# Optimization experiments

Measured on AMD Instinct MI355X. Metric: run time of the kernel, lower is better.

## Reference

```python
import jax, jax.numpy as jnp
import numpy as np

B, T, N, H = 256, 256, 512, 512  # batch, seq_len, input_size, hidden_size_encoder


def setup_inputs() -> dict:
    key = jax.random.key(0)
    k = jax.random.split(key, 9)
    return {
        "input_data": jax.random.normal(k[0], (B, T, N), dtype=jnp.float32),
        # init_hidden uses xavier_normal on zeros -> random init; std ~ sqrt(2/(B+H))
        "h0": jax.random.normal(k[1], (B, H), dtype=jnp.float32) * 0.06,
        "c0": jax.random.normal(k[2], (B, H), dtype=jnp.float32) * 0.06,
        # attn Linear: in_features = 2H + T, out_features = 1
        "attn_w": jax.random.normal(k[3], (2 * H + T,), dtype=jnp.float32) * 0.02,
        "attn_b": jnp.zeros((), dtype=jnp.float32),
        # single-layer LSTM params (torch gate order: i, f, g, o)
        "w_ih": jax.random.normal(k[4], (4 * H, N), dtype=jnp.float32) * 0.02,
        "w_hh": jax.random.normal(k[5], (4 * H, H), dtype=jnp.float32) * 0.02,
        "b_ih": jax.random.normal(k[6], (4 * H,), dtype=jnp.float32) * 0.02,
        "b_hh": jax.random.normal(k[7], (4 * H,), dtype=jnp.float32) * 0.02,
    }


def reference(input_data, h0, c0, attn_w, attn_b, w_ih, w_hh, b_ih, b_hh):
    Bd, Td, Nd = input_data.shape
    Hd = h0.shape[-1]
    # split attn weight into h-, c-, and x-parts (same math as the concat+Linear)
    w_h, w_c, w_x = attn_w[:Hd], attn_w[Hd:2 * Hd], attn_w[2 * Hd:]
    # x-part of the attention logits is time-invariant: [B, N]
    proj_x = jnp.einsum('btn,t->bn', input_data, w_x)
    b_gate = b_ih + b_hh  # [4H]

    def step(carry, x_t):  # x_t: [B, N]
        h, c = carry
        # attention logits: broadcast h/c contribution over the N input series
        e = proj_x + (h @ w_h)[:, None] + (c @ w_c)[:, None] + attn_b  # [B, N]
        a = jax.nn.softmax(e, axis=1)  # softmax over input_size dim
        weighted = a * x_t  # [B, N]
        gates = weighted @ w_ih.T + h @ w_hh.T + b_gate  # [B, 4H]
        i_g, f_g, g_g, o_g = jnp.split(gates, 4, axis=1)
        i_g = jax.nn.sigmoid(i_g)
        f_g = jax.nn.sigmoid(f_g)
        g_g = jnp.tanh(g_g)
        o_g = jax.nn.sigmoid(o_g)
        c_new = f_g * c + i_g * g_g
        h_new = o_g * jnp.tanh(c_new)
        return (h_new, c_new), (a, h_new)

    xs = jnp.swapaxes(input_data, 0, 1)  # [T, B, N]
    _, (attn_seq, enc_seq) = jax.lax.scan(step, (h0, c0), xs)
    attentions = jnp.swapaxes(attn_seq, 0, 1)      # [B, T, N]
    input_encoded = jnp.swapaxes(enc_seq, 0, 1)    # [B, T, H]
    return attentions, input_encoded
```

## Files before the change

kernel.cpp:

```cpp
#include <hip/hip_runtime.h>

#define BB 256
#define TT 256
#define NN 512
#define HH 512

typedef short short8 __attribute__((ext_vector_type(8)));
typedef float f32x4 __attribute__((ext_vector_type(4)));
typedef unsigned long long u64;

static __device__ __forceinline__ ushort f2bf(float f) {
  uint b = __builtin_bit_cast(uint, f);
  b += 0x7FFFu + ((b >> 16) & 1u);
  return (ushort)(b >> 16);
}
static __device__ __forceinline__ uint pk2(float lo, float hi) {
  return (uint)f2bf(lo) | ((uint)f2bf(hi) << 16);
}
static __device__ __forceinline__ float sigm_(float x) {
  return 1.0f / (1.0f + exp2f(-1.4426950408889634f * x));
}
static __device__ __forceinline__ float tanh_(float x) {
  return 2.0f / (1.0f + exp2f(-2.8853900817779268f * x)) - 1.0f;
}
static __device__ __forceinline__ void bar_lds() {
  asm volatile("s_waitcnt lgkmcnt(0)" ::: "memory");
  __builtin_amdgcn_s_barrier();
}

__global__ __launch_bounds__(256) void prep_kernel(
    const float* __restrict__ w_ih, const float* __restrict__ w_hh,
    const float* __restrict__ b_ih, const float* __restrict__ b_hh,
    const float* __restrict__ h0,
    ushort* __restrict__ W2, float* __restrict__ bgate,
    uint* __restrict__ hx16a, unsigned* __restrict__ bar) {
  int idx = blockIdx.x * 256 + threadIdx.x;
  if (idx < 2048 * 1024) {
    int row = idx >> 10;
    int k = idx & 1023;
    float v = (k < NN) ? w_ih[row * NN + k] : w_hh[row * HH + (k - NN)];
    W2[idx] = f2bf(v);
  }
  if (idx < 2048) bgate[idx] = b_ih[idx] + b_hh[idx];
  if (idx < BB * HH / 2) hx16a[idx] = pk2(h0[2 * idx], h0[2 * idx + 1]);
  if (idx < 16 * 64) bar[idx] = 0u;
}

__global__ __launch_bounds__(256) void attn_kernel(
    const float* __restrict__ x, const float* __restrict__ attn_w,
    float* __restrict__ a_out, ushort* __restrict__ ax) {
  __shared__ float wx[TT];
  __shared__ float as[NN];
  __shared__ float red[8];
  const int b = blockIdx.x;
  const int tid = threadIdx.x;
  wx[tid] = attn_w[2 * HH + tid];
  __syncthreads();

  const float* xb = x + (size_t)b * TT * NN;
  float p0 = 0.0f, p1 = 0.0f;
  for (int t = 0; t < TT; ++t) {
    float w = wx[t];
    p0 += xb[t * NN + tid] * w;
    p1 += xb[t * NN + 256 + tid] * w;
  }

  const int lane = tid & 63, wv = tid >> 6;
  float m = fmaxf(p0, p1);
  #pragma unroll
  for (int o = 32; o; o >>= 1) m = fmaxf(m, __shfl_xor(m, o));
  if (lane == 0) red[wv] = m;
  __syncthreads();
  m = fmaxf(fmaxf(red[0], red[1]), fmaxf(red[2], red[3]));
  float e0 = expf(p0 - m), e1 = expf(p1 - m);
  float s = e0 + e1;
  #pragma unroll
  for (int o = 32; o; o >>= 1) s += __shfl_xor(s, o);
  if (lane == 0) red[4 + wv] = s;
  __syncthreads();
  s = red[4] + red[5] + red[6] + red[7];
  float inv = 1.0f / s;
  float a0 = e0 * inv, a1 = e1 * inv;
  a_out[b * NN + tid] = a0;
  a_out[b * NN + 256 + tid] = a1;
  as[tid] = a0;
  as[tid + 256] = a1;
  __syncthreads();

  const float aa0 = as[tid * 2], aa1 = as[tid * 2 + 1];
  ushort* axb = ax + (size_t)b * TT * NN;
  for (int t = 0; t < TT; ++t) {
    const float2 xv = *(const float2*)(xb + t * NN + tid * 2);
    *(uint*)(axb + t * NN + tid * 2) = pk2(aa0 * xv.x, aa1 * xv.y);
  }
}

__global__ __launch_bounds__(256) void bcast_kernel(
    const float* __restrict__ a, float* __restrict__ attn_out) {
  const size_t idx = (size_t)blockIdx.x * 256 + threadIdx.x;
  const int n4 = (int)(idx & 127);
  const int t = (int)((idx >> 7) & 255);
  const int b = (int)(idx >> 15);
  const float4 v = *(const float4*)(a + b * NN + n4 * 4);
  *(float4*)(attn_out + (((size_t)b * TT + t) * NN + n4 * 4)) = v;
}

__global__ __launch_bounds__(512, 2) void lstm_persistent(
    const ushort* __restrict__ ax,
    const ushort* __restrict__ W2,
    const float* __restrict__ bgate,
    const float* __restrict__ c0,
    uint* __restrict__ hx16a, uint* __restrict__ hx16b,
    float* __restrict__ enc,
    unsigned* __restrict__ bar) {
  __shared__ ushort hx[16 * 1024];
  __shared__ unsigned warr;
  __shared__ unsigned step_flag;

  const int tid = threadIdx.x;
  const int lane = tid & 63;
  const int w = tid >> 6;
  const int bg = blockIdx.x & 15;
  const int jt = blockIdx.x >> 4;
  const int gb0 = bg * 16;
  unsigned* const barp = bar + bg * 64;

  if (tid == 0) { warr = 0u; step_flag = 0u; }

  f32x4 areg[32];
  {
    const int r = lane & 15;
    const int grow = (r & 3) * 512 + jt * 32 + w * 4 + (r >> 2);
    const ushort* wp = W2 + (size_t)grow * 1024 + ((lane >> 4) << 3);
    #pragma unroll
    for (int i = 0; i < 32; ++i) {
      areg[i] = *(const f32x4*)(wp + (i << 5));
      asm volatile("" : "+v"(areg[i]));
    }
  }

  const int srow = tid >> 5;
  const int sl = tid & 31;
  const int r7 = srow & 7;

  const int eb = lane & 15;
  const int kq = lane >> 4;
  const int ecol = jt * 32 + w * 4 + kq;
  const float bgi = bgate[ecol];
  const float bgf = bgate[512 + ecol];
  const float bgg = bgate[1024 + ecol];
  const float bgo = bgate[1536 + ecol];
  float c_reg = c0[(size_t)(gb0 + eb) * HH + ecol];

  const int bbase = (lane & 15) * 1024;
  const int br7 = (lane & 15) & 7;

  uint4 px0, px1;
  {
    const ushort* axp = ax + ((size_t)(gb0 + srow) * TT + 0) * NN;
    px0 = *(const uint4*)(axp + sl * 8);
    px1 = *(const uint4*)(axp + 256 + sl * 8);
  }

  for (int t = 0; t < TT; ++t) {
    const uint* hin = (t & 1) ? hx16b : hx16a;
    uint* hout = (t & 1) ? hx16a : hx16b;

    *(uint4*)&hx[srow * 1024 + ((sl ^ r7) << 3)] = px0;
    *(uint4*)&hx[srow * 1024 + (((32 + sl) ^ r7) << 3)] = px1;
    if (t + 1 < TT) {
      const ushort* axp = ax + ((size_t)(gb0 + srow) * TT + (t + 1)) * NN;
      px0 = *(const uint4*)(axp + sl * 8);
      px1 = *(const uint4*)(axp + 256 + sl * 8);
    }
    bar_lds();

    f32x4 acc = {0.f, 0.f, 0.f, 0.f};
    u64 q0, q1, q2, q3;
    const uint* hrow = hin + (size_t)(gb0 + srow) * 256;

    auto xmfma = [&]() {
      #pragma unroll
      for (int ks = 0; ks < 16; ++ks) {
        const int ag = ks * 4 + kq;
        const short8 bf = *(const short8*)&hx[bbase + ((ag ^ br7) << 3)];
        acc = __builtin_amdgcn_mfma_f32_16x16x32_bf16(
            __builtin_bit_cast(short8, areg[ks]), bf, acc, 0, 0, 0);
      }
    };
    auto hload = [&]() {
      q0 = __hip_atomic_load((const u64*)(hrow + sl * 4),
                             __ATOMIC_RELAXED, __HIP_MEMORY_SCOPE_AGENT);
      q1 = __hip_atomic_load((const u64*)(hrow + sl * 4 + 2),
                             __ATOMIC_RELAXED, __HIP_MEMORY_SCOPE_AGENT);
      q2 = __hip_atomic_load((const u64*)(hrow + 128 + sl * 4),
                             __ATOMIC_RELAXED, __HIP_MEMORY_SCOPE_AGENT);
      q3 = __hip_atomic_load((const u64*)(hrow + 128 + sl * 4 + 2),
                             __ATOMIC_RELAXED, __HIP_MEMORY_SCOPE_AGENT);
    };

    if (t == 0) {
      hload();
      xmfma();
    } else if (w == 0) {
      if (lane == 0) {
        const unsigned target = 16u * (unsigned)t;
        while (__hip_atomic_load(barp, __ATOMIC_RELAXED,
                                 __HIP_MEMORY_SCOPE_AGENT) < target)
          __builtin_amdgcn_s_sleep(1);
        __hip_atomic_store(&step_flag, (unsigned)t, __ATOMIC_RELEASE,
                           __HIP_MEMORY_SCOPE_WORKGROUP);
      }
      asm volatile("" ::: "memory");
      hload();
      xmfma();
    } else {
      xmfma();
      if (lane == 0) {
        while (__hip_atomic_load(&step_flag, __ATOMIC_ACQUIRE,
                                 __HIP_MEMORY_SCOPE_WORKGROUP) < (unsigned)t) {}
      }
      asm volatile("" ::: "memory");
      hload();
    }

    {
      uint4 p0, p1;
      p0.x = (uint)q0; p0.y = (uint)(q0 >> 32);
      p0.z = (uint)q1; p0.w = (uint)(q1 >> 32);
      p1.x = (uint)q2; p1.y = (uint)(q2 >> 32);
      p1.z = (uint)q3; p1.w = (uint)(q3 >> 32);
      *(uint4*)&hx[srow * 1024 + (((64 + sl) ^ r7) << 3)] = p0;
      *(uint4*)&hx[srow * 1024 + (((96 + sl) ^ r7) << 3)] = p1;
    }
    bar_lds();

    #pragma unroll
    for (int ks = 16; ks < 32; ++ks) {
      const int ag = ks * 4 + kq;
      const short8 bf = *(const short8*)&hx[bbase + ((ag ^ br7) << 3)];
      acc = __builtin_amdgcn_mfma_f32_16x16x32_bf16(
          __builtin_bit_cast(short8, areg[ks]), bf, acc, 0, 0, 0);
    }

    {
      const float ig = sigm_(acc[0] + bgi);
      const float fg = sigm_(acc[1] + bgf);
      const float gg = tanh_(acc[2] + bgg);
      const float og = sigm_(acc[3] + bgo);
      const float cn = fg * c_reg + ig * gg;
      const float hn = og * tanh_(cn);
      c_reg = cn;
      const float hp_ = __shfl_xor(hn, 16);
      if (!(lane & 16)) {
        __hip_atomic_store(hout + (size_t)(gb0 + eb) * 256 + (ecol >> 1),
                           pk2(hn, hp_),
                           __ATOMIC_RELAXED, __HIP_MEMORY_SCOPE_AGENT);
      }
      asm volatile("s_waitcnt vmcnt(0)" ::: "memory");
      if (lane == 0) {
        const unsigned old = __hip_atomic_fetch_add(
            &warr, 1u, __ATOMIC_ACQ_REL, __HIP_MEMORY_SCOPE_WORKGROUP);
        if (old == 8u * (unsigned)t + 7u)
          __hip_atomic_fetch_add(barp, 1u, __ATOMIC_RELAXED,
                                 __HIP_MEMORY_SCOPE_AGENT);
      }
      enc[((size_t)(gb0 + eb) * TT + t) * HH + ecol] = hn;
    }
  }
}

extern "C" void kernel_launch(void* const* d_in, const int* in_sizes, int n_in,
                              void* d_out, int out_size, void* d_ws, size_t ws_size,
                              hipStream_t stream) {
  const float* x      = (const float*)d_in[0];
  const float* h0     = (const float*)d_in[1];
  const float* c0     = (const float*)d_in[2];
  const float* attn_w = (const float*)d_in[3];
  const float* w_ih   = (const float*)d_in[5];
  const float* w_hh   = (const float*)d_in[6];
  const float* b_ih   = (const float*)d_in[7];
  const float* b_hh   = (const float*)d_in[8];

  float* attn_out = (float*)d_out;
  float* enc_out  = (float*)d_out + (size_t)BB * TT * NN;
  ushort* ax = (ushort*)d_out;

  char* ws = (char*)d_ws;
  float*    a_ws  = (float*)(ws);
  ushort*   W2_ws = (ushort*)(ws + 0x80000);
  float*    bg_ws = (float*)(ws + 0x480000);
  uint*     hx16a = (uint*)(ws + 0x482000);
  uint*     hx16b = (uint*)(ws + 0x4C2000);
  unsigned* bar   = (unsigned*)(ws + 0x502000);

  prep_kernel<<<8192, 256, 0, stream>>>(w_ih, w_hh, b_ih, b_hh, h0,
                                        W2_ws, bg_ws, hx16a, bar);
  attn_kernel<<<BB, 256, 0, stream>>>(x, attn_w, a_ws, ax);

  {
    dim3 grid(256), block(512);
    void* args[] = {(void*)&ax, (void*)&W2_ws, (void*)&bg_ws, (void*)&c0,
                    (void*)&hx16a, (void*)&hx16b, (void*)&enc_out,
                    (void*)&bar};
    hipLaunchCooperativeKernel((void*)lstm_persistent, grid, block, args, 0,
                               stream);
  }

  bcast_kernel<<<32768, 256, 0, stream>>>(a_ws, attn_out);
}
```

Measured before the change: 833.2 us.

## Double-buffer LDS x tile to drop per-step barrier and split x-MFMA around h wait

Measured after the change: 1.220 ms. 46.5% more time.

```diff
diff --git a/kernel.cpp b/kernel.cpp
--- a/kernel.cpp
+++ b/kernel.cpp
@@ -113,7 +113,7 @@
     uint* __restrict__ hx16a, uint* __restrict__ hx16b,
     float* __restrict__ enc,
     unsigned* __restrict__ bar) {
-  __shared__ ushort hx[16 * 1024];
+  __shared__ ushort hx[2][16 * 1024];
   __shared__ unsigned warr;
   __shared__ unsigned step_flag;
 
@@ -124,8 +124,6 @@
   const int jt = blockIdx.x >> 4;
   const int gb0 = bg * 16;
   unsigned* const barp = bar + bg * 64;
-
-  if (tid == 0) { warr = 0u; step_flag = 0u; }
 
   f32x4 areg[32];
   {
@@ -158,70 +156,74 @@
   uint4 px0, px1;
   {
     const ushort* axp = ax + ((size_t)(gb0 + srow) * TT + 0) * NN;
-    px0 = *(const uint4*)(axp + sl * 8);
-    px1 = *(const uint4*)(axp + 256 + sl * 8);
-  }
+    const uint4 a0 = *(const uint4*)(axp + sl * 8);
+    const uint4 a1 = *(const uint4*)(axp + 256 + sl * 8);
+    *(uint4*)&hx[0][srow * 1024 + ((sl ^ r7) << 3)] = a0;
+    *(uint4*)&hx[0][srow * 1024 + (((32 + sl) ^ r7) << 3)] = a1;
+    const ushort* axp1 = ax + ((size_t)(gb0 + srow) * TT + 1) * NN;
+    px0 = *(const uint4*)(axp1 + sl * 8);
+    px1 = *(const uint4*)(axp1 + 256 + sl * 8);
+  }
+  if (tid == 0) { warr = 0u; step_flag = 0u; }
+  __syncthreads();
 
   for (int t = 0; t < TT; ++t) {
+    ushort* const bufp = &hx[t & 1][0];
+    ushort* const bufn = &hx[(t & 1) ^ 1][0];
     const uint* hin = (t & 1) ? hx16b : hx16a;
     uint* hout = (t & 1) ? hx16a : hx16b;
-
-    *(uint4*)&hx[srow * 1024 + ((sl ^ r7) << 3)] = px0;
-    *(uint4*)&hx[srow * 1024 + (((32 + sl) ^ r7) << 3)] = px1;
-    if (t + 1 < TT) {
-      const ushort* axp = ax + ((size_t)(gb0 + srow) * TT + (t + 1)) * NN;
-      px0 = *(const uint4*)(axp + sl * 8);
-      px1 = *(const uint4*)(axp + 256 + sl * 8);
-    }
-    bar_lds();
+    const uint* hrow = hin + (size_t)(gb0 + srow) * 256;
 
     f32x4 acc = {0.f, 0.f, 0.f, 0.f};
-    u64 q0, q1, q2, q3;
-    const uint* hrow = hin + (size_t)(gb0 + srow) * 256;
-
-    auto xmfma = [&]() {
-      #pragma unroll
-      for (int ks = 0; ks < 16; ++ks) {
-        const int ag = ks * 4 + kq;
-        const short8 bf = *(const short8*)&hx[bbase + ((ag ^ br7) << 3)];
-        acc = __builtin_amdgcn_mfma_f32_16x16x32_bf16(
-            __builtin_bit_cast(short8, areg[ks]), bf, acc, 0, 0, 0);
-      }
-    };
-    auto hload = [&]() {
-      q0 = __hip_atomic_load((const u64*)(hrow + sl * 4),
-                             __ATOMIC_RELAXED, __HIP_MEMORY_SCOPE_AGENT);
-      q1 = __hip_atomic_load((const u64*)(hrow + sl * 4 + 2),
-                             __ATOMIC_RELAXED, __HIP_MEMORY_SCOPE_AGENT);
-      q2 = __hip_atomic_load((const u64*)(hrow + 128 + sl * 4),
-                             __ATOMIC_RELAXED, __HIP_MEMORY_SCOPE_AGENT);
-      q3 = __hip_atomic_load((const u64*)(hrow + 128 + sl * 4 + 2),
-                             __ATOMIC_RELAXED, __HIP_MEMORY_SCOPE_AGENT);
-    };
-
-    if (t == 0) {
-      hload();
-      xmfma();
-    } else if (w == 0) {
-      if (lane == 0) {
-        const unsigned target = 16u * (unsigned)t;
-        while (__hip_atomic_load(barp, __ATOMIC_RELAXED,
-                                 __HIP_MEMORY_SCOPE_AGENT) < target)
-          __builtin_amdgcn_s_sleep(1);
-        __hip_atomic_store(&step_flag, (unsigned)t, __ATOMIC_RELEASE,
-                           __HIP_MEMORY_SCOPE_WORKGROUP);
+
+    #pragma unroll
+    for (int ks = 0; ks < 8; ++ks) {
+      const int ag = ks * 4 + kq;
+      const short8 bf = *(const short8*)&bufp[bbase + ((ag ^ br7) << 3)];
+      acc = __builtin_amdgcn_mfma_f32_16x16x32_bf16(
+          __builtin_bit_cast(short8, areg[ks]), bf, acc, 0, 0, 0);
+    }
+
+    if (t) {
+      if (w == 0) {
+        if (lane == 0) {
+          const unsigned target = 16u * (unsigned)t;
+          while (__hip_atomic_load(barp, __ATOMIC_RELAXED,
+                                   __HIP_MEMORY_SCOPE_AGENT) < target)
+            __builtin_amdgcn_s_sleep(1);
+          __hip_atomic_store(&step_flag, (unsigned)t, __ATOMIC_RELEASE,
+                             __HIP_MEMORY_SCOPE_WORKGROUP);
+        }
+      } else {
+        if (lane == 0) {
+          while (__hip_atomic_load(&step_flag, __ATOMIC_ACQUIRE,
+                                   __HIP_MEMORY_SCOPE_WORKGROUP) < (unsigned)t) {}
+        }
       }
       asm volatile("" ::: "memory");
-      hload();
-      xmfma();
-    } else {
-      xmfma();
-      if (lane == 0) {
-        while (__hip_atomic_load(&step_flag, __ATOMIC_ACQUIRE,
-                                 __HIP_MEMORY_SCOPE_WORKGROUP) < (unsigned)t) {}
-      }
-      asm volatile("" ::: "memory");
-      hload();
+    }
+
+    u64 q0, q1, q2, q3;
+    q0 = __hip_atomic_load((const u64*)(hrow + sl * 4),
+                           __ATOMIC_RELAXED, __HIP_MEMORY_SCOPE_AGENT);
+    q1 = __hip_atomic_load((const u64*)(hrow + sl * 4 + 2),
+                           __ATOMIC_RELAXED, __HIP_MEMORY_SCOPE_AGENT);
+    q2 = __hip_atomic_load((const u64*)(hrow + 128 + sl * 4),
+                           __ATOMIC_RELAXED, __HIP_MEMORY_SCOPE_AGENT);
+    q3 = __hip_atomic_load((const u64*)(hrow + 128 + sl * 4 + 2),
+                           __ATOMIC_RELAXED, __HIP_MEMORY_SCOPE_AGENT);
+
+    #pragma unroll
+    for (int ks = 8; ks < 16; ++ks) {
+      const int ag = ks * 4 + kq;
+      const short8 bf = *(const short8*)&bufp[bbase + ((ag ^ br7) << 3)];
+      acc = __builtin_amdgcn_mfma_f32_16x16x32_bf16(
+          __builtin_bit_cast(short8, areg[ks]), bf, acc, 0, 0, 0);
+    }
+
+    if (t + 1 < TT) {
+      *(uint4*)&bufn[srow * 1024 + ((sl ^ r7) << 3)] = px0;
+      *(uint4*)&bufn[srow * 1024 + (((32 + sl) ^ r7) << 3)] = px1;
     }
 
     {
@@ -230,15 +232,22 @@
       p0.z = (uint)q1; p0.w = (uint)(q1 >> 32);
       p1.x = (uint)q2; p1.y = (uint)(q2 >> 32);
       p1.z = (uint)q3; p1.w = (uint)(q3 >> 32);
-      *(uint4*)&hx[srow * 1024 + (((64 + sl) ^ r7) << 3)] = p0;
-      *(uint4*)&hx[srow * 1024 + (((96 + sl) ^ r7) << 3)] = p1;
-    }
+      *(uint4*)&bufp[srow * 1024 + (((64 + sl) ^ r7) << 3)] = p0;
+      *(uint4*)&bufp[srow * 1024 + (((96 + sl) ^ r7) << 3)] = p1;
+    }
+
+    if (t + 2 < TT) {
+      const ushort* axp = ax + ((size_t)(gb0 + srow) * TT + (t + 2)) * NN;
+      px0 = *(const uint4*)(axp + sl * 8);
+      px1 = *(const uint4*)(axp + 256 + sl * 8);
+    }
+
     bar_lds();
 
     #pragma unroll
     for (int ks = 16; ks < 32; ++ks) {
       const int ag = ks * 4 + kq;
-      const short8 bf = *(const short8*)&hx[bbase + ((ag ^ br7) << 3)];
+      const short8 bf = *(const short8*)&bufp[bbase + ((ag ^ br7) << 3)];
       acc = __builtin_amdgcn_mfma_f32_16x16x32_bf16(
           __builtin_bit_cast(short8, areg[ks]), bf, acc, 0, 0, 0);
     }
```
